# Kernel tuning notes

Hardware: AMD Instinct MI355X
Metric: run time of the kernel (lower is better)

Reference implementation:

```python
import jax, jax.numpy as jnp
import numpy as np

N, E, F_IN, D_COORD, W, KW, KIN, DEPTH = 10000, 300000, 3, 3, 32, 256, 6, 4

def _lin(k, i, o):
    return jax.random.normal(k, (i, o), jnp.float32) * (1.0 / np.sqrt(i))

def setup_inputs() -> dict:
    key = jax.random.key(0)
    ks = jax.random.split(key, 16)
    x = jax.random.normal(ks[0], (N, F_IN), jnp.float32)
    edge_index = jax.random.randint(ks[1], (2, E), 0, N, jnp.int64)
    edge_attr = jax.random.normal(ks[2], (E, KIN), jnp.float32)
    coords_init = jax.random.normal(ks[3], (N, D_COORD), jnp.float32)
    return {
        "x": x, "edge_index": edge_index, "edge_attr": edge_attr,
        "coords_init": coords_init,
        "fc1_w": _lin(ks[4], F_IN, W), "fc1_b": jnp.zeros((W,), jnp.float32),
        # kernel DenseNet: [ker_in, ker_width//2, ker_width, width**2]
        "ker1_w": _lin(ks[5], KIN, KW // 2), "ker1_b": jnp.zeros((KW // 2,), jnp.float32),
        "ker2_w": _lin(ks[6], KW // 2, KW), "ker2_b": jnp.zeros((KW,), jnp.float32),
        "ker3_w": _lin(ks[7], KW, W * W), "ker3_b": jnp.zeros((W * W,), jnp.float32),
        # coord MLP: Linear(W,W)+ReLU+Linear(W,1)
        "cm1_w": _lin(ks[8], W, W), "cm1_b": jnp.zeros((W,), jnp.float32),
        "cm2_w": _lin(ks[9], W, 1), "cm2_b": jnp.zeros((1,), jnp.float32),
        # fc2: Linear(W,2W)+ReLU+Linear(2W,1)
        "fc2a_w": _lin(ks[10], W, 2 * W), "fc2a_b": jnp.zeros((2 * W,), jnp.float32),
        "fc2b_w": _lin(ks[11], 2 * W, 1), "fc2b_b": jnp.zeros((1,), jnp.float32),
        "depth": DEPTH,
    }

def reference(x, edge_index, edge_attr, coords_init,
              fc1_w, fc1_b, ker1_w, ker1_b, ker2_w, ker2_b, ker3_w, ker3_b,
              cm1_w, cm1_b, cm2_w, cm2_b, fc2a_w, fc2a_b, fc2b_w, fc2b_b, depth):
    n = x.shape[0]
    w = fc1_w.shape[1]
    row, col = edge_index[0], edge_index[1]
    h = x @ fc1_w + fc1_b  # [N, W]
    # edge kernel MLP -> per-edge [W, W] matrix (edge_attr fixed across layers)
    k = jax.nn.relu(edge_attr @ ker1_w + ker1_b)
    k = jax.nn.relu(k @ ker2_w + ker2_b)
    k = (k @ ker3_w + ker3_b).reshape(-1, w, w)  # [E, W, W]
    cnt = jnp.clip(jax.ops.segment_sum(jnp.ones((row.shape[0], 1), h.dtype), row, n), 1.0)
    coord = coords_init
    for _ in range(depth):
        m = jnp.einsum('eij,ej->ei', k, h[col])              # gather + kernel apply
        agg = jax.ops.segment_sum(m, row, n) / cnt           # mean scatter to nodes
        we = jax.nn.relu(m @ cm1_w + cm1_b) @ cm2_w + cm2_b  # [E, 1] coord weights
        trans = (coord[row] - coord[col]) * we               # equivariant edge vectors
        coord = coord + jax.ops.segment_sum(trans, row, n) / cnt
        h = jax.nn.relu(h + agg)
    out = jax.nn.relu(h @ fc2a_w + fc2a_b) @ fc2b_w + fc2b_b  # [N, 1]
    return out, coord
```

## Files before the change

### kernel.cpp

```cpp
#include <hip/hip_runtime.h>

#define NN 10000
#define NE 300000
#define DEPTH 4

typedef unsigned int   u32;
typedef unsigned short u16;
typedef unsigned char  u8;

typedef _Float16 half8  __attribute__((ext_vector_type(8)));
typedef _Float16 half2t __attribute__((ext_vector_type(2)));
typedef float  floatx16 __attribute__((ext_vector_type(16)));

__device__ __forceinline__ u32 f2h(float f) {
    f = fminf(fmaxf(f, -60000.f), 60000.f);
    _Float16 h = (_Float16)f;
    return (u32)__builtin_bit_cast(u16, h);
}
__device__ __forceinline__ float h2f(u16 b) {
    return (float)__builtin_bit_cast(_Float16, b);
}

__global__ void sentinel_kernel(float* out, int n, float val) {
    int i = blockIdx.x * 256 + threadIdx.x;
    if (i < n) out[i] = val;
}

__global__ void detect_idx_kernel(const int* __restrict__ ei, int* __restrict__ flag) {
    __shared__ int nz;
    if (threadIdx.x == 0) nz = 0;
    __syncthreads();
    if (ei[threadIdx.x * 2 + 1] != 0) atomicAdd(&nz, 1);
    __syncthreads();
    if (threadIdx.x == 0) *flag = (nz == 0) ? 1 : 0;
}

__global__ __launch_bounds__(256) void convert_idx_kernel(
    const int* __restrict__ ei, const int* __restrict__ flag,
    int* __restrict__ ridx, int* __restrict__ cidx)
{
    int e = blockIdx.x * 256 + threadIdx.x;
    if (e >= 2 * NE) return;
    const int is64 = *flag;
    int v = is64 ? ei[2 * e] : ei[e];
    if (e < NE) ridx[e] = v; else cidx[e - NE] = v;
}

__global__ __launch_bounds__(256) void init_nodes_kernel(
    const float* __restrict__ x, const float* __restrict__ fc1w,
    const float* __restrict__ fc1b, const float* __restrict__ ci,
    float* __restrict__ h, float* __restrict__ coord)
{
    int idx = blockIdx.x * 256 + threadIdx.x;
    if (idx < NN * 32) {
        int v = idx >> 5, f = idx & 31;
        float acc = fc1b[f];
#pragma unroll
        for (int i = 0; i < 3; i++) acc += x[v * 3 + i] * fc1w[i * 32 + f];
        h[idx] = acc;
    }
    if (idx < NN * 3) coord[idx] = ci[idx];
}

__global__ __launch_bounds__(256) void count_kernel(
    const int* __restrict__ ridx, const int* __restrict__ cidx,
    int* __restrict__ rowcnt, int* __restrict__ colcnt)
{
    int e = blockIdx.x * 256 + threadIdx.x;
    if (e < NE) { atomicAdd(&rowcnt[ridx[e]], 1); atomicAdd(&colcnt[cidx[e]], 1); }
}

__global__ void scan_kernel(const int* __restrict__ colcnt, const int* __restrict__ rowcnt,
                            int* __restrict__ cstart, int* __restrict__ cnext,
                            int* __restrict__ rstart, int* __restrict__ rnext,
                            float* __restrict__ invc, int mode)
{
    __shared__ int partC[256], partR[256];
    const int t = threadIdx.x;
    int sumC = 0, sumR = 0;
    for (int i = 0; i < 40; i++) {
        int v = t * 40 + i;
        if (v < NN) { sumC += colcnt[v]; sumR += rowcnt[v]; }
    }
    partC[t] = sumC; partR[t] = sumR;
    __syncthreads();
    if (t == 0) {
        int rc = 0, rr = 0;
        for (int i = 0; i < 256; i++) {
            int tc = partC[i]; partC[i] = rc; rc += tc;
            int tr = partR[i]; partR[i] = rr; rr += tr;
        }
    }
    __syncthreads();
    int runC = partC[t], runR = partR[t];
    for (int i = 0; i < 40; i++) {
        int v = t * 40 + i;
        if (v < NN) {
            cstart[v] = runC; cnext[v] = runC; runC += colcnt[v];
            if (mode) { rstart[v] = runR; rnext[v] = runR; runR += rowcnt[v]; }
        }
    }
    if (t == 255) { cstart[NN] = runC; if (mode) rstart[NN] = runR; }
    for (int v = t; v < NN; v += 256) invc[v] = 1.0f / fmaxf((float)rowcnt[v], 1.0f);
}

__global__ __launch_bounds__(256) void scatter_kernel(
    const int* __restrict__ cidx, const int* __restrict__ ridx,
    int* __restrict__ cnext, int* __restrict__ rnext,
    int* __restrict__ elist, int* __restrict__ rpos, int* __restrict__ rcol,
    int mode)
{
    int e = blockIdx.x * 256 + threadIdx.x;
    if (e >= NE) return;
    int pos = atomicAdd(&cnext[cidx[e]], 1);
    elist[pos] = e;
    if (mode) {
        int rp = atomicAdd(&rnext[ridx[e]], 1);
        rpos[e] = rp;
        rcol[rp] = cidx[e];
    }
}

__global__ __launch_bounds__(256) void w2pack_kernel(
    const float* __restrict__ w2, u16* __restrict__ w2h)
{
    const int slot = blockIdx.x * 256 + threadIdx.x;
    const int c = slot >> 9, s = (slot >> 6) & 7, l = slot & 63;
    const int li = l & 31, hf = l >> 5;
    const int k0 = s * 16 + hf * 8, col = c * 32 + li;
    u32 pk[8];
#pragma unroll
    for (int j = 0; j < 8; j++) pk[j] = f2h(w2[(size_t)(k0 + j) * 256 + col]);
    uint4 o;
    o.x = pk[0] | (pk[1] << 16);
    o.y = pk[2] | (pk[3] << 16);
    o.z = pk[4] | (pk[5] << 16);
    o.w = pk[6] | (pk[7] << 16);
    *(uint4*)&w2h[(size_t)slot * 8] = o;
}

__global__ void cm1pack_kernel(const float* __restrict__ cm1w, u16* __restrict__ cmpk)
{
    const int t = threadIdx.x;
    if (t >= 128) return;
    const int s2 = t >> 6, l = t & 63, li = l & 31, hf = l >> 5;
    u32 pk[8];
#pragma unroll
    for (int j = 0; j < 8; j++) pk[j] = f2h(cm1w[(s2 * 16 + hf * 8 + j) * 32 + li]);
    uint4 o;
    o.x = pk[0] | (pk[1] << 16);
    o.y = pk[2] | (pk[3] << 16);
    o.z = pk[4] | (pk[5] << 16);
    o.w = pk[6] | (pk[7] << 16);
    *(uint4*)&cmpk[(size_t)(s2 * 64 + l) * 8] = o;
}

__global__ __launch_bounds__(256) void mlp_k2_kernel(
    const float* __restrict__ ea,
    const float* __restrict__ w1, const float* __restrict__ b1,
    const u16* __restrict__ w2h, const float* __restrict__ b2,
    u8* __restrict__ k2base, float* __restrict__ k2s)
{
    __shared__ __align__(16) float ea_s[32 * 6];
    __shared__ __align__(16) u16   k1f[4096];
    __shared__ __align__(16) u16   M_s[32 * 258];
    __shared__ float pmax_s[4][32];
    const int t  = threadIdx.x;
    const int e0 = blockIdx.x * 32;

    for (int idx = t; idx < 192; idx += 256)
        ea_s[idx] = ea[(size_t)e0 * 6 + idx];
    __syncthreads();

    for (int slot = t; slot < 512; slot += 256) {
        const int s  = slot >> 6;
        const int l  = slot & 63;
        const int li = l & 31, hf = l >> 5;
        const int k0 = s * 16 + hf * 8;
        float acc[8];
        {
            const float4 ba = *(const float4*)&b1[k0];
            const float4 bb = *(const float4*)&b1[k0 + 4];
            acc[0] = ba.x; acc[1] = ba.y; acc[2] = ba.z; acc[3] = ba.w;
            acc[4] = bb.x; acc[5] = bb.y; acc[6] = bb.z; acc[7] = bb.w;
        }
#pragma unroll
        for (int i = 0; i < 6; i++) {
            const float ev = ea_s[li * 6 + i];
            const float4 wa = *(const float4*)&w1[i * 128 + k0];
            const float4 wb = *(const float4*)&w1[i * 128 + k0 + 4];
            acc[0] += ev * wa.x; acc[1] += ev * wa.y;
            acc[2] += ev * wa.z; acc[3] += ev * wa.w;
            acc[4] += ev * wb.x; acc[5] += ev * wb.y;
            acc[6] += ev * wb.z; acc[7] += ev * wb.w;
        }
        uint4 o;
        o.x = f2h(fmaxf(acc[0], 0.f)) | (f2h(fmaxf(acc[1], 0.f)) << 16);
        o.y = f2h(fmaxf(acc[2], 0.f)) | (f2h(fmaxf(acc[3], 0.f)) << 16);
        o.z = f2h(fmaxf(acc[4], 0.f)) | (f2h(fmaxf(acc[5], 0.f)) << 16);
        o.w = f2h(fmaxf(acc[6], 0.f)) | (f2h(fmaxf(acc[7], 0.f)) << 16);
        *(uint4*)&k1f[slot * 8] = o;
    }
    __syncthreads();

    {
        const int w  = t >> 6, l = t & 63;
        const int li = l & 31, hf = l >> 5;
#pragma unroll
        for (int ct = 0; ct < 2; ct++) {
            const int c = w * 2 + ct;
            floatx16 acc;
#pragma unroll
            for (int r = 0; r < 16; r++) acc[r] = 0.f;
#pragma unroll
            for (int s = 0; s < 8; s++) {
                const half8 a = __builtin_bit_cast(half8,
                    *(const uint4*)&k1f[(s * 64 + l) * 8]);
                const half8 b = __builtin_bit_cast(half8,
                    *(const uint4*)&w2h[(((size_t)c * 8 + s) * 64 + l) * 8]);
                acc = __builtin_amdgcn_mfma_f32_32x32x16_f16(a, b, acc, 0, 0, 0);
            }
            const float bb = b2[c * 32 + li];
#pragma unroll
            for (int r = 0; r < 16; r++) {
                const int e = (r & 3) + 8 * (r >> 2) + 4 * hf;
                M_s[e * 258 + c * 32 + li] = (u16)f2h(fmaxf(acc[r] + bb, 0.f));
            }
        }
    }
    __syncthreads();

    {
        const int el = t & 31, qq = t >> 5;
        const int w  = t >> 6;
        float vals[32];
#pragma unroll
        for (int c = 0; c < 16; c++) {
            const u32 hw = *(const u32*)&M_s[el * 258 + qq * 32 + c * 2];
            vals[c * 2]     = h2f((u16)hw);
            vals[c * 2 + 1] = h2f((u16)(hw >> 16));
        }
        float mx = 0.f;
#pragma unroll
        for (int u = 0; u < 32; u++) mx = fmaxf(mx, vals[u]);
        mx = fmaxf(mx, __shfl_xor(mx, 32, 64));
        if ((t & 32) == 0) pmax_s[w][el] = mx;
        __syncthreads();
        mx = fmaxf(fmaxf(pmax_s[0][el], pmax_s[1][el]),
                   fmaxf(pmax_s[2][el], pmax_s[3][el]));
        const float sc  = mx / 255.f;
        const float inv = (mx > 0.f) ? 255.f / mx : 0.f;
        if (t < 32) k2s[e0 + el] = sc;
        u32 w8[8];
#pragma unroll
        for (int u = 0; u < 8; u++) {
            u32 q0 = (u32)fminf(rintf(vals[u * 4 + 0] * inv), 255.f);
            u32 q1 = (u32)fminf(rintf(vals[u * 4 + 1] * inv), 255.f);
            u32 q2 = (u32)fminf(rintf(vals[u * 4 + 2] * inv), 255.f);
            u32 q3 = (u32)fminf(rintf(vals[u * 4 + 3] * inv), 255.f);
            w8[u] = q0 | (q1 << 8) | (q2 << 16) | (q3 << 24);
        }
        u8* outp = k2base + (size_t)(e0 + el) * 256 + qq * 32;
        *(uint4*)outp        = make_uint4(w8[0], w8[1], w8[2], w8[3]);
        *(uint4*)(outp + 16) = make_uint4(w8[4], w8[5], w8[6], w8[7]);
    }
}

__global__ __launch_bounds__(256) void bvec_kernel(
    const float* __restrict__ h, const float* __restrict__ b3, float* __restrict__ bvec)
{
    int idx = blockIdx.x * 256 + threadIdx.x;
    if (idx >= NN * 32) return;
    int v = idx >> 5, i = idx & 31;
    const float* hp = &h[(size_t)v * 32];
    const float* bp = &b3[i * 32];
    float acc = 0.f;
#pragma unroll
    for (int c = 0; c < 8; c++) {
        float4 hv = *(const float4*)&hp[c * 4];
        float4 bv = *(const float4*)&bp[c * 4];
        acc += hv.x * bv.x + hv.y * bv.y + hv.z * bv.z + hv.w * bv.w;
    }
    bvec[idx] = acc;
}

__global__ __launch_bounds__(256) void g_kernel(
    const float* __restrict__ h, const float* __restrict__ w3,
    u16* __restrict__ Gg)
{
    __shared__ __align__(16) u32 h16[128 * 16];
    const int t  = threadIdx.x;
    const int v0 = blockIdx.x * 128;

    {
        const int v = t >> 1, hh = t & 1;
        float4 a = make_float4(0.f, 0.f, 0.f, 0.f), b = a, c = a, d = a;
        if (v0 + v < NN) {
            const float* hp = &h[(size_t)(v0 + v) * 32 + hh * 16];
            a = *(const float4*)hp;       b = *(const float4*)(hp + 4);
            c = *(const float4*)(hp + 8); d = *(const float4*)(hp + 12);
        }
        uint4 o0, o1;
        o0.x = f2h(a.x) | (f2h(a.y) << 16);
        o0.y = f2h(a.z) | (f2h(a.w) << 16);
        o0.z = f2h(b.x) | (f2h(b.y) << 16);
        o0.w = f2h(b.z) | (f2h(b.w) << 16);
        o1.x = f2h(c.x) | (f2h(c.y) << 16);
        o1.y = f2h(c.z) | (f2h(c.w) << 16);
        o1.z = f2h(d.x) | (f2h(d.y) << 16);
        o1.w = f2h(d.z) | (f2h(d.w) << 16);
        *(uint4*)&h16[v * 16 + hh * 8]     = o0;
        *(uint4*)&h16[v * 16 + hh * 8 + 4] = o1;
    }
    __syncthreads();

    const int by    = blockIdx.y;
    const int lane  = t >> 2;
    const int i     = lane & 31;
    const int halfk = lane >> 5;
    const int j0    = (t & 3) * 2;
    const int k0    = by * 16 + halfk * 8 + j0;

    u32 w0p[16], w1p[16];
    {
        const float* wp0 = &w3[(size_t)k0 * 1024 + (size_t)i * 32];
        const float* wp1 = wp0 + 1024;
#pragma unroll
        for (int c = 0; c < 8; c++) {
            const float4 a = *(const float4*)&wp0[c * 4];
            w0p[c * 2]     = f2h(a.x) | (f2h(a.y) << 16);
            w0p[c * 2 + 1] = f2h(a.z) | (f2h(a.w) << 16);
            const float4 b = *(const float4*)&wp1[c * 4];
            w1p[c * 2]     = f2h(b.x) | (f2h(b.y) << 16);
            w1p[c * 2 + 1] = f2h(b.z) | (f2h(b.w) << 16);
        }
    }
    const int vmax = min(128, NN - v0);
    u32* outp = (u32*)Gg;
#pragma unroll 2
    for (int v = 0; v < vmax; v++) {
        float a0 = 0.f, a1 = 0.f;
#pragma unroll
        for (int c = 0; c < 4; c++) {
            const uint4 q = *(const uint4*)&h16[v * 16 + c * 4];
            const half2t h0 = __builtin_bit_cast(half2t, q.x);
            const half2t h1 = __builtin_bit_cast(half2t, q.y);
            const half2t h2 = __builtin_bit_cast(half2t, q.z);
            const half2t h3 = __builtin_bit_cast(half2t, q.w);
            a0 = __builtin_amdgcn_fdot2(h0, __builtin_bit_cast(half2t, w0p[c*4+0]), a0, false);
            a0 = __builtin_amdgcn_fdot2(h1, __builtin_bit_cast(half2t, w0p[c*4+1]), a0, false);
            a0 = __builtin_amdgcn_fdot2(h2, __builtin_bit_cast(half2t, w0p[c*4+2]), a0, false);
            a0 = __builtin_amdgcn_fdot2(h3, __builtin_bit_cast(half2t, w0p[c*4+3]), a0, false);
            a1 = __builtin_amdgcn_fdot2(h0, __builtin_bit_cast(half2t, w1p[c*4+0]), a1, false);
            a1 = __builtin_amdgcn_fdot2(h1, __builtin_bit_cast(half2t, w1p[c*4+1]), a1, false);
            a1 = __builtin_amdgcn_fdot2(h2, __builtin_bit_cast(half2t, w1p[c*4+2]), a1, false);
            a1 = __builtin_amdgcn_fdot2(h3, __builtin_bit_cast(half2t, w1p[c*4+3]), a1, false);
        }
        outp[(size_t)(v0 + v) * 4096 + by * 256 + t] = f2h(a0) | (f2h(a1) << 16);
    }
}

__global__ __launch_bounds__(256) void edge_kernel(
    const int* __restrict__ cstart, const int* __restrict__ elist,
    const int* __restrict__ ridx, const int* __restrict__ rpos,
    const u8* __restrict__ k2base, const float* __restrict__ k2s,
    const u16* __restrict__ Gg, const float* __restrict__ coord,
    const u16* __restrict__ cmpk, const float* __restrict__ cm1b,
    const float* __restrict__ cm2w, const float* __restrict__ cm2b,
    const float* __restrict__ bvec,
    float* __restrict__ agg, float* __restrict__ dco,
    u16* __restrict__ mbuf, u16* __restrict__ webuf, int mode)
{
    const int t    = threadIdx.x;
    const int w    = t >> 6;
    const int l    = t & 63;
    const int li   = l & 31;
    const int half = l >> 5;

    __shared__ __align__(16) float Mlds_all[4][32 * 34];
    __shared__ int idxS_all[4][32];
    float* Mlds = Mlds_all[w];
    int*   idxS = idxS_all[w];

    const int n = blockIdx.x * 4 + w;
    if (n >= NN) return;
    const int s0  = cstart[n];
    const int deg = cstart[n + 1] - s0;
    if (deg == 0) return;

    half8 cmb[2];
    cmb[0] = __builtin_bit_cast(half8, *(const uint4*)&cmpk[(size_t)(0 * 64 + l) * 8]);
    cmb[1] = __builtin_bit_cast(half8, *(const uint4*)&cmpk[(size_t)(1 * 64 + l) * 8]);
    half8 onesb;
#pragma unroll
    for (int j = 0; j < 8; j++) onesb[j] = (_Float16)1.0f;
    const float cm1bq = cm1b[li];
    const float cm2q  = cm2w[li];
    const float cm2b0 = cm2b[0];
    const float bv    = bvec[n * 32 + li];
    const float con   = (mode == 0 && li < 3) ? coord[(size_t)n * 3 + li] : 0.f;
    const u16* Gn = Gg + (size_t)n * 8192;

    for (int base = 0; base < deg; base += 32) {
        const int mye   = base + li;
        const int valid = (mye < deg) ? 1 : 0;
        const int eid   = valid ? elist[s0 + mye] : 0;
        if (l < 32) idxS[l] = valid ? (mode ? rpos[eid] : ridx[eid]) : 0;

        uint4 gr[16];
#pragma unroll
        for (int s = 0; s < 16; s++)
            gr[s] = *(const uint4*)(Gn + s * 512 + l * 8);
        const float se = valid ? k2s[eid] : 0.f;
        const u8* k2row = k2base + (size_t)eid * 256 + half * 8;
        uint2 kr[16];
#pragma unroll
        for (int s = 0; s < 16; s++) kr[s] = *(const uint2*)(k2row + s * 16);

        floatx16 acc;
#pragma unroll
        for (int r = 0; r < 16; r++) acc[r] = bv;
#pragma unroll
        for (int s = 0; s < 16; s++) {
            half8 a;
#pragma unroll
            for (int j = 0; j < 4; j++) {
                a[j]     = (_Float16)((float)((kr[s].x >> (8 * j)) & 0xffu) * se);
                a[4 + j] = (_Float16)((float)((kr[s].y >> (8 * j)) & 0xffu) * se);
            }
            acc = __builtin_amdgcn_mfma_f32_32x32x16_f16(
                a, __builtin_bit_cast(half8, gr[s]), acc, 0, 0, 0);
        }

#pragma unroll
        for (int r = 0; r < 16; r++) {
            const int e = (r & 3) + 8 * (r >> 2) + 4 * half;
            Mlds[e * 34 + li] = acc[r];
        }
        if (mode == 0) {
#pragma unroll
            for (int r = 0; r < 16; r++) {
                const int e = (r & 3) + 8 * (r >> 2) + 4 * half;
                if (base + e < deg)
                    atomicAdd(&agg[(size_t)idxS[e] * 32 + li], acc[r]);
            }
        } else {
#pragma unroll
            for (int r = 0; r < 16; r++) {
                const int e = (r & 3) + 8 * (r >> 2) + 4 * half;
                if (base + e < deg)
                    mbuf[(size_t)idxS[e] * 32 + li] = (u16)f2h(acc[r]);
            }
        }
        asm volatile("s_waitcnt lgkmcnt(0)" ::: "memory");

        floatx16 acc2;
#pragma unroll
        for (int r = 0; r < 16; r++) acc2[r] = cm1bq;
#pragma unroll
        for (int s2 = 0; s2 < 2; s2++) {
            const float* mp = &Mlds[li * 34 + s2 * 16 + half * 8];
            const float2 m0 = *(const float2*)mp;
            const float2 m1 = *(const float2*)(mp + 2);
            const float2 m2 = *(const float2*)(mp + 4);
            const float2 m3 = *(const float2*)(mp + 6);
            half8 a;
            a[0] = (_Float16)m0.x; a[1] = (_Float16)m0.y;
            a[2] = (_Float16)m1.x; a[3] = (_Float16)m1.y;
            a[4] = (_Float16)m2.x; a[5] = (_Float16)m2.y;
            a[6] = (_Float16)m3.x; a[7] = (_Float16)m3.y;
            acc2 = __builtin_amdgcn_mfma_f32_32x32x16_f16(a, cmb[s2], acc2, 0, 0, 0);
        }

#pragma unroll
        for (int r = 0; r < 16; r++) {
            const int e = (r & 3) + 8 * (r >> 2) + 4 * half;
            Mlds[e * 34 + li] = fmaxf(acc2[r], 0.f) * cm2q;
        }
        asm volatile("s_waitcnt lgkmcnt(0)" ::: "memory");
        floatx16 acc3;
#pragma unroll
        for (int r = 0; r < 16; r++) acc3[r] = cm2b0;
#pragma unroll
        for (int s2 = 0; s2 < 2; s2++) {
            const float* mp = &Mlds[li * 34 + s2 * 16 + half * 8];
            const float2 m0 = *(const float2*)mp;
            const float2 m1 = *(const float2*)(mp + 2);
            const float2 m2 = *(const float2*)(mp + 4);
            const float2 m3 = *(const float2*)(mp + 6);
            half8 a;
            a[0] = (_Float16)m0.x; a[1] = (_Float16)m0.y;
            a[2] = (_Float16)m1.x; a[3] = (_Float16)m1.y;
            a[4] = (_Float16)m2.x; a[5] = (_Float16)m2.y;
            a[6] = (_Float16)m3.x; a[7] = (_Float16)m3.y;
            acc3 = __builtin_amdgcn_mfma_f32_32x32x16_f16(a, onesb, acc3, 0, 0, 0);
        }

        if (mode == 0) {
#pragma unroll
            for (int r = 0; r < 16; r++) {
                const int e = (r & 3) + 8 * (r >> 2) + 4 * half;
                if (base + e < deg && li < 3) {
                    const int rr = idxS[e];
                    const float d = coord[(size_t)rr * 3 + li] - con;
                    atomicAdd(&dco[(size_t)rr * 3 + li], d * acc3[r]);
                }
            }
        } else {
#pragma unroll
            for (int r = 0; r < 16; r++) {
                const int e = (r & 3) + 8 * (r >> 2) + 4 * half;
                if (base + e < deg && li == 0)
                    webuf[idxS[e]] = (u16)f2h(acc3[r]);
            }
        }
    }
}

__global__ __launch_bounds__(256) void node_update_kernel(
    float* __restrict__ h, float* __restrict__ agg,
    float* __restrict__ coord, float* __restrict__ dco,
    const float* __restrict__ invc)
{
    int idx = blockIdx.x * 256 + threadIdx.x;
    if (idx < NN * 32) {
        int v = idx >> 5;
        h[idx] = fmaxf(h[idx] + agg[idx] * invc[v], 0.f);
        agg[idx] = 0.f;
    }
    if (idx < NN * 3) {
        coord[idx] += dco[idx] * invc[idx / 3];
        dco[idx] = 0.f;
    }
}

__global__ __launch_bounds__(256) void node_update2_kernel(
    float* __restrict__ h, const float* __restrict__ coordCur,
    float* __restrict__ coordNew, const u16* __restrict__ mbuf,
    const u16* __restrict__ webuf, const int* __restrict__ rcol,
    const int* __restrict__ rstart, const float* __restrict__ invc)
{
    const int t = threadIdx.x, w = t >> 6, l = t & 63;
    const int li = l & 31, half = l >> 5;
    const int v = blockIdx.x * 4 + w;
    if (v >= NN) return;
    const int s0 = rstart[v], s1 = rstart[v + 1];
    const float iv = invc[v];

    float acc = 0.f;
    for (int s = s0 + half; s < s1; s += 2)
        acc += h2f(mbuf[(size_t)s * 32 + li]);
    acc += __shfl_xor(acc, 32, 64);
    if (half == 0)
        h[(size_t)v * 32 + li] = fmaxf(h[(size_t)v * 32 + li] + acc * iv, 0.f);

    const float c0 = coordCur[(size_t)v * 3 + 0];
    const float c1 = coordCur[(size_t)v * 3 + 1];
    const float c2 = coordCur[(size_t)v * 3 + 2];
    float p0 = 0.f, p1 = 0.f, p2 = 0.f;
    for (int s = s0 + l; s < s1; s += 64) {
        const float we = h2f(webuf[s]);
        const int col = rcol[s];
        p0 += (c0 - coordCur[(size_t)col * 3 + 0]) * we;
        p1 += (c1 - coordCur[(size_t)col * 3 + 1]) * we;
        p2 += (c2 - coordCur[(size_t)col * 3 + 2]) * we;
    }
#pragma unroll
    for (int off = 32; off >= 1; off >>= 1) {
        p0 += __shfl_xor(p0, off, 64);
        p1 += __shfl_xor(p1, off, 64);
        p2 += __shfl_xor(p2, off, 64);
    }
    if (l == 0) {
        coordNew[(size_t)v * 3 + 0] = c0 + p0 * iv;
        coordNew[(size_t)v * 3 + 1] = c1 + p1 * iv;
        coordNew[(size_t)v * 3 + 2] = c2 + p2 * iv;
    }
}

__global__ __launch_bounds__(256) void final_kernel(
    const float* __restrict__ h, const float* __restrict__ coord,
    const float* __restrict__ wa, const float* __restrict__ ba,
    const float* __restrict__ wb, const float* __restrict__ bb,
    float* __restrict__ out)
{
    const int lane = threadIdx.x & 63;
    const int v = blockIdx.x * 4 + (threadIdx.x >> 6);
    if (v >= NN) return;
    const float hreg = (lane < 32) ? h[(size_t)v * 32 + lane] : 0.f;
    float acc = ba[lane];
#pragma unroll
    for (int f = 0; f < 32; f++) acc += __shfl(hreg, f, 64) * wa[f * 64 + lane];
    float part = fmaxf(acc, 0.f) * wb[lane];
#pragma unroll
    for (int off = 32; off >= 1; off >>= 1) part += __shfl_xor(part, off, 64);
    if (lane == 0) out[v] = part + bb[0];
    if (lane < 3) out[NN + (size_t)v * 3 + lane] = coord[(size_t)v * 3 + lane];
}

extern "C" void kernel_launch(void* const* d_in, const int* in_sizes, int n_in,
                              void* d_out, int out_size, void* d_ws, size_t ws_size,
                              hipStream_t stream)
{
    const float* x    = (const float*)d_in[0];
    const int*   ei   = (const int*)d_in[1];
    const float* ea   = (const float*)d_in[2];
    const float* ci   = (const float*)d_in[3];
    const float* fc1w = (const float*)d_in[4];
    const float* fc1b = (const float*)d_in[5];
    const float* k1w  = (const float*)d_in[6];
    const float* k1b  = (const float*)d_in[7];
    const float* k2w  = (const float*)d_in[8];
    const float* k2b  = (const float*)d_in[9];
    const float* k3w  = (const float*)d_in[10];
    const float* k3b  = (const float*)d_in[11];
    const float* cm1w = (const float*)d_in[12];
    const float* cm1b = (const float*)d_in[13];
    const float* cm2w = (const float*)d_in[14];
    const float* cm2b = (const float*)d_in[15];
    const float* f2aw = (const float*)d_in[16];
    const float* f2ab = (const float*)d_in[17];
    const float* f2bw = (const float*)d_in[18];
    const float* f2bb = (const float*)d_in[19];

    size_t o_k2, o_k2s, o_G, o_h, o_bv, o_coA, o_coB, o_invc, o_rc, o_cc,
           o_cs, o_rs, o_cn, o_rn, o_el, o_w2h, o_cmpk, o_agg, o_dco,
           o_ri, o_ci, o_rp, o_rcl, o_mb, o_wb;
#define ALGN(v) (((v) + 255) & ~(size_t)255)
    auto carve = [&](int mode) -> size_t {
        size_t o = 0;
        o_k2  = o; o += ALGN((size_t)NE * 256);
        o_k2s = o; o += ALGN((size_t)NE * 4);
        o_G   = o; o += ALGN((size_t)NN * 8192 * 2);
        o_h   = o; o += ALGN((size_t)NN * 32 * 4);
        o_bv  = o; o += ALGN((size_t)NN * 32 * 4);
        o_coA = o; o += ALGN((size_t)NN * 3 * 4);
        o_invc= o; o += ALGN((size_t)NN * 4);
        o_rc  = o; o += ALGN((size_t)NN * 4);
        o_cc  = o; o += ALGN((size_t)NN * 4);
        o_cs  = o; o += ALGN((size_t)(NN + 1) * 4);
        o_cn  = o; o += ALGN((size_t)NN * 4);
        o_el  = o; o += ALGN((size_t)NE * 4);
        o_w2h = o; o += ALGN((size_t)128 * 256 * 2);
        o_cmpk= o; o += ALGN((size_t)1024 * 2);
        if (mode == 0) {
            o_agg = o; o += ALGN((size_t)NN * 32 * 4);
            o_dco = o; o += ALGN((size_t)NN * 3 * 4);
            o_ri  = o; o += ALGN((size_t)NE * 4);
            o_ci  = o; o += ALGN((size_t)NE * 4);
            o_coB = o_coA; o_rs = o_cs; o_rn = o_cn;
            o_rp = o_el; o_rcl = o_el; o_mb = o_k2; o_wb = o_k2;
        } else {
            o_coB = o; o += ALGN((size_t)NN * 3 * 4);
            o_rs  = o; o += ALGN((size_t)(NN + 1) * 4);
            o_rn  = o; o += ALGN((size_t)NN * 4);
            o_rp  = o; o += ALGN((size_t)NE * 4);
            o_rcl = o; o += ALGN((size_t)NE * 4);
            const size_t u = o;
            o_ri = u; o_ci = u + ALGN((size_t)NE * 4);
            o_mb = u; o_wb = u + ALGN((size_t)NE * 32 * 2);
            const size_t setup_sz = 2 * ALGN((size_t)NE * 4);
            const size_t layer_sz = ALGN((size_t)NE * 32 * 2) + ALGN((size_t)NE * 2);
            o += (setup_sz > layer_sz) ? setup_sz : layer_sz;
            o_agg = o_k2; o_dco = o_k2;
        }
        return o;
    };
    int mode = (ws_size >= carve(1)) ? 1 : 0;
    size_t need = carve(mode);
    if (ws_size < need) {
        sentinel_kernel<<<(NN * 4 + 255) / 256, 256, 0, stream>>>((float*)d_out, NN * 4, 1.0e6f);
        return;
    }

    char* wsb = (char*)d_ws;
    u8*    k2g   = (u8*)(wsb + o_k2);
    float* k2s   = (float*)(wsb + o_k2s);
    u16*   Gg    = (u16*)(wsb + o_G);
    float* h     = (float*)(wsb + o_h);
    float* bvec  = (float*)(wsb + o_bv);
    float* coA   = (float*)(wsb + o_coA);
    float* coB   = (float*)(wsb + o_coB);
    float* invc  = (float*)(wsb + o_invc);
    int*   rowcnt= (int*)(wsb + o_rc);
    int*   colcnt= (int*)(wsb + o_cc);
    int*   cstart= (int*)(wsb + o_cs);
    int*   rstart= (int*)(wsb + o_rs);
    int*   cnext = (int*)(wsb + o_cn);
    int*   rnext = (int*)(wsb + o_rn);
    int*   elist = (int*)(wsb + o_el);
    u16*   w2h   = (u16*)(wsb + o_w2h);
    u16*   cmpk  = (u16*)(wsb + o_cmpk);
    float* agg   = (float*)(wsb + o_agg);
    float* dco   = (float*)(wsb + o_dco);
    int*   ridx  = (int*)(wsb + o_ri);
    int*   cidx  = (int*)(wsb + o_ci);
    int*   rpos  = (int*)(wsb + o_rp);
    int*   rcol  = (int*)(wsb + o_rcl);
    u16*   mbuf  = (u16*)(wsb + o_mb);
    u16*   webuf = (u16*)(wsb + o_wb);

    hipMemsetAsync(rowcnt, 0, (size_t)NN * 4, stream);
    hipMemsetAsync(colcnt, 0, (size_t)NN * 4, stream);
    if (mode == 0) {
        hipMemsetAsync(agg, 0, (size_t)NN * 32 * 4, stream);
        hipMemsetAsync(dco, 0, (size_t)NN * 3 * 4, stream);
    }

    detect_idx_kernel<<<1, 256, 0, stream>>>(ei, cnext);
    convert_idx_kernel<<<(2 * NE + 255) / 256, 256, 0, stream>>>(ei, cnext, ridx, cidx);
    init_nodes_kernel<<<(NN * 32 + 255) / 256, 256, 0, stream>>>(x, fc1w, fc1b, ci, h, coA);
    count_kernel<<<(NE + 255) / 256, 256, 0, stream>>>(ridx, cidx, rowcnt, colcnt);
    scan_kernel<<<1, 256, 0, stream>>>(colcnt, rowcnt, cstart, cnext, rstart, rnext,
                                       invc, mode);
    scatter_kernel<<<(NE + 255) / 256, 256, 0, stream>>>(cidx, ridx, cnext, rnext,
                                                         elist, rpos, rcol, mode);
    w2pack_kernel<<<16, 256, 0, stream>>>(k2w, w2h);
    cm1pack_kernel<<<1, 128, 0, stream>>>(cm1w, cmpk);
    mlp_k2_kernel<<<NE / 32, 256, 0, stream>>>(ea, k1w, k1b, w2h, k2b, k2g, k2s);

    float* coCur = coA;
    float* coAlt = coB;
    const dim3 ggrid((NN + 127) / 128, 16);
    for (int l = 0; l < DEPTH; l++) {
        bvec_kernel<<<(NN * 32 + 255) / 256, 256, 0, stream>>>(h, k3b, bvec);
        g_kernel<<<ggrid, 256, 0, stream>>>(h, k3w, Gg);
        edge_kernel<<<(NN + 3) / 4, 256, 0, stream>>>(cstart, elist, ridx, rpos,
                                                      k2g, k2s, Gg, coCur, cmpk,
                                                      cm1b, cm2w, cm2b, bvec,
                                                      agg, dco, mbuf, webuf, mode);
        if (mode == 1) {
            node_update2_kernel<<<(NN + 3) / 4, 256, 0, stream>>>(
                h, coCur, coAlt, mbuf, webuf, rcol, rstart, invc);
            float* tmp = coCur; coCur = coAlt; coAlt = tmp;
        } else {
            node_update_kernel<<<(NN * 32 + 255) / 256, 256, 0, stream>>>(
                h, agg, coCur, dco, invc);
        }
    }
    final_kernel<<<(NN + 3) / 4, 256, 0, stream>>>(h, coCur, f2aw, f2ab, f2bw, f2bb,
                                                   (float*)d_out);
}
```

Measured before the change: 924.7 us.

## Use MFMA for per-node G projection and cheaper fp16 dequant in edge kernel

```diff
diff --git a/kernel.cpp b/kernel.cpp
--- a/kernel.cpp
+++ b/kernel.cpp
@@ -19,6 +19,14 @@
 }
 __device__ __forceinline__ float h2f(u16 b) {
     return (float)__builtin_bit_cast(_Float16, b);
+}
+__device__ __forceinline__ u32 pkrtz2(float a, float b) {
+    return __builtin_bit_cast(u32, __builtin_amdgcn_cvt_pkrtz(a, b));
+}
+__device__ __forceinline__ u32 dq2(u32 x, u32 sel) {
+    const half2t h1024 = {(_Float16)1024.f, (_Float16)1024.f};
+    half2t v = __builtin_bit_cast(half2t, __builtin_amdgcn_perm(x, 0x64646464u, sel));
+    return __builtin_bit_cast(u32, v - h1024);
 }
 
 __global__ void sentinel_kernel(float* out, int n, float val) {
@@ -155,11 +163,36 @@
     *(uint4*)&cmpk[(size_t)(s2 * 64 + l) * 8] = o;
 }
 
+__global__ __launch_bounds__(256) void w3pack_kernel(
+    const float* __restrict__ w3, u16* __restrict__ w3g)
+{
+    const int slot = blockIdx.x * 256 + threadIdx.x;
+    const int lane = slot & 63;
+    const int ks   = (slot >> 6) & 1;
+    const int pt   = slot >> 7;
+    const int p    = pt * 32 + (lane & 31);
+    const int kb   = ks * 16 + (lane >> 5) * 8;
+    const int s  = p >> 9;
+    const int hf = (p >> 8) & 1;
+    const int i  = (p >> 3) & 31;
+    const int j7 = p & 7;
+    const int c  = s * 16 + hf * 8 + j7;
+    const float* wp = &w3[(size_t)c * 1024 + i * 32 + kb];
+    const float4 x0 = *(const float4*)wp;
+    const float4 x1 = *(const float4*)(wp + 4);
+    uint4 o;
+    o.x = f2h(x0.x) | (f2h(x0.y) << 16);
+    o.y = f2h(x0.z) | (f2h(x0.w) << 16);
+    o.z = f2h(x1.x) | (f2h(x1.y) << 16);
+    o.w = f2h(x1.z) | (f2h(x1.w) << 16);
+    *(uint4*)&w3g[(size_t)slot * 8] = o;
+}
+
 __global__ __launch_bounds__(256) void mlp_k2_kernel(
     const float* __restrict__ ea,
     const float* __restrict__ w1, const float* __restrict__ b1,
     const u16* __restrict__ w2h, const float* __restrict__ b2,
-    u8* __restrict__ k2base, float* __restrict__ k2s)
+    u8* __restrict__ k2base, u16* __restrict__ k2s)
 {
     __shared__ __align__(16) float ea_s[32 * 6];
     __shared__ __align__(16) u16   k1f[4096];
@@ -195,10 +228,10 @@
             acc[6] += ev * wb.z; acc[7] += ev * wb.w;
         }
         uint4 o;
-        o.x = f2h(fmaxf(acc[0], 0.f)) | (f2h(fmaxf(acc[1], 0.f)) << 16);
-        o.y = f2h(fmaxf(acc[2], 0.f)) | (f2h(fmaxf(acc[3], 0.f)) << 16);
-        o.z = f2h(fmaxf(acc[4], 0.f)) | (f2h(fmaxf(acc[5], 0.f)) << 16);
-        o.w = f2h(fmaxf(acc[6], 0.f)) | (f2h(fmaxf(acc[7], 0.f)) << 16);
+        o.x = pkrtz2(fmaxf(acc[0], 0.f), fmaxf(acc[1], 0.f));
+        o.y = pkrtz2(fmaxf(acc[2], 0.f), fmaxf(acc[3], 0.f));
+        o.z = pkrtz2(fmaxf(acc[4], 0.f), fmaxf(acc[5], 0.f));
+        o.w = pkrtz2(fmaxf(acc[6], 0.f), fmaxf(acc[7], 0.f));
         *(uint4*)&k1f[slot * 8] = o;
     }
     __syncthreads();
@@ -224,7 +257,8 @@
 #pragma unroll
             for (int r = 0; r < 16; r++) {
                 const int e = (r & 3) + 8 * (r >> 2) + 4 * hf;
-                M_s[e * 258 + c * 32 + li] = (u16)f2h(fmaxf(acc[r] + bb, 0.f));
+                M_s[e * 258 + c * 32 + li] =
+                    __builtin_bit_cast(u16, (_Float16)fmaxf(acc[r] + bb, 0.f));
             }
         }
     }
@@ -250,7 +284,7 @@
                    fmaxf(pmax_s[2][el], pmax_s[3][el]));
         const float sc  = mx / 255.f;
         const float inv = (mx > 0.f) ? 255.f / mx : 0.f;
-        if (t < 32) k2s[e0 + el] = sc;
+        if (t < 32) k2s[e0 + el] = (u16)f2h(sc);
         u32 w8[8];
 #pragma unroll
         for (int u = 0; u < 8; u++) {
@@ -285,85 +319,69 @@
 }
 
 __global__ __launch_bounds__(256) void g_kernel(
-    const float* __restrict__ h, const float* __restrict__ w3,
+    const float* __restrict__ h, const u16* __restrict__ w3g,
     u16* __restrict__ Gg)
 {
-    __shared__ __align__(16) u32 h16[128 * 16];
-    const int t  = threadIdx.x;
-    const int v0 = blockIdx.x * 128;
-
-    {
-        const int v = t >> 1, hh = t & 1;
-        float4 a = make_float4(0.f, 0.f, 0.f, 0.f), b = a, c = a, d = a;
-        if (v0 + v < NN) {
-            const float* hp = &h[(size_t)(v0 + v) * 32 + hh * 16];
-            a = *(const float4*)hp;       b = *(const float4*)(hp + 4);
-            c = *(const float4*)(hp + 8); d = *(const float4*)(hp + 12);
-        }
-        uint4 o0, o1;
-        o0.x = f2h(a.x) | (f2h(a.y) << 16);
-        o0.y = f2h(a.z) | (f2h(a.w) << 16);
-        o0.z = f2h(b.x) | (f2h(b.y) << 16);
-        o0.w = f2h(b.z) | (f2h(b.w) << 16);
-        o1.x = f2h(c.x) | (f2h(c.y) << 16);
-        o1.y = f2h(c.z) | (f2h(c.w) << 16);
-        o1.z = f2h(d.x) | (f2h(d.y) << 16);
-        o1.w = f2h(d.z) | (f2h(d.w) << 16);
-        *(uint4*)&h16[v * 16 + hh * 8]     = o0;
-        *(uint4*)&h16[v * 16 + hh * 8 + 4] = o1;
-    }
-    __syncthreads();
-
-    const int by    = blockIdx.y;
-    const int lane  = t >> 2;
-    const int i     = lane & 31;
-    const int halfk = lane >> 5;
-    const int j0    = (t & 3) * 2;
-    const int k0    = by * 16 + halfk * 8 + j0;
-
-    u32 w0p[16], w1p[16];
-    {
-        const float* wp0 = &w3[(size_t)k0 * 1024 + (size_t)i * 32];
-        const float* wp1 = wp0 + 1024;
-#pragma unroll
-        for (int c = 0; c < 8; c++) {
-            const float4 a = *(const float4*)&wp0[c * 4];
-            w0p[c * 2]     = f2h(a.x) | (f2h(a.y) << 16);
-            w0p[c * 2 + 1] = f2h(a.z) | (f2h(a.w) << 16);
-            const float4 b = *(const float4*)&wp1[c * 4];
-            w1p[c * 2]     = f2h(b.x) | (f2h(b.y) << 16);
-            w1p[c * 2 + 1] = f2h(b.z) | (f2h(b.w) << 16);
-        }
-    }
-    const int vmax = min(128, NN - v0);
-    u32* outp = (u32*)Gg;
-#pragma unroll 2
-    for (int v = 0; v < vmax; v++) {
-        float a0 = 0.f, a1 = 0.f;
-#pragma unroll
-        for (int c = 0; c < 4; c++) {
-            const uint4 q = *(const uint4*)&h16[v * 16 + c * 4];
-            const half2t h0 = __builtin_bit_cast(half2t, q.x);
-            const half2t h1 = __builtin_bit_cast(half2t, q.y);
-            const half2t h2 = __builtin_bit_cast(half2t, q.z);
-            const half2t h3 = __builtin_bit_cast(half2t, q.w);
-            a0 = __builtin_amdgcn_fdot2(h0, __builtin_bit_cast(half2t, w0p[c*4+0]), a0, false);
-            a0 = __builtin_amdgcn_fdot2(h1, __builtin_bit_cast(half2t, w0p[c*4+1]), a0, false);
-            a0 = __builtin_amdgcn_fdot2(h2, __builtin_bit_cast(half2t, w0p[c*4+2]), a0, false);
-            a0 = __builtin_amdgcn_fdot2(h3, __builtin_bit_cast(half2t, w0p[c*4+3]), a0, false);
-            a1 = __builtin_amdgcn_fdot2(h0, __builtin_bit_cast(half2t, w1p[c*4+0]), a1, false);
-            a1 = __builtin_amdgcn_fdot2(h1, __builtin_bit_cast(half2t, w1p[c*4+1]), a1, false);
-            a1 = __builtin_amdgcn_fdot2(h2, __builtin_bit_cast(half2t, w1p[c*4+2]), a1, false);
-            a1 = __builtin_amdgcn_fdot2(h3, __builtin_bit_cast(half2t, w1p[c*4+3]), a1, false);
-        }
-        outp[(size_t)(v0 + v) * 4096 + by * 256 + t] = f2h(a0) | (f2h(a1) << 16);
+    const int t = threadIdx.x, w = t >> 6, l = t & 63;
+    const int li = l & 31, hf = l >> 5;
+    const int n0 = blockIdx.x * 32;
+    const int node = n0 + li;
+
+    half8 a0, a1;
+    if (node < NN) {
+        const float* hp = &h[(size_t)node * 32 + hf * 8];
+        const float4 x0 = *(const float4*)hp;
+        const float4 x1 = *(const float4*)(hp + 4);
+        const float4 y0 = *(const float4*)(hp + 16);
+        const float4 y1 = *(const float4*)(hp + 20);
+        uint4 ua, ub;
+        ua.x = pkrtz2(x0.x, x0.y); ua.y = pkrtz2(x0.z, x0.w);
+        ua.z = pkrtz2(x1.x, x1.y); ua.w = pkrtz2(x1.z, x1.w);
+        ub.x = pkrtz2(y0.x, y0.y); ub.y = pkrtz2(y0.z, y0.w);
+        ub.z = pkrtz2(y1.x, y1.y); ub.w = pkrtz2(y1.z, y1.w);
+        a0 = __builtin_bit_cast(half8, ua);
+        a1 = __builtin_bit_cast(half8, ub);
+    } else {
+        const uint4 z = make_uint4(0u, 0u, 0u, 0u);
+        a0 = __builtin_bit_cast(half8, z);
+        a1 = __builtin_bit_cast(half8, z);
+    }
+
+    const int pt0 = blockIdx.y * 64 + w * 16;
+    const int full = (n0 + 32 <= NN) ? 1 : 0;
+#pragma unroll 4
+    for (int it = 0; it < 16; it++) {
+        const int pt = pt0 + it;
+        const uint4 b0u = *(const uint4*)&w3g[((size_t)pt * 2 + 0) * 512 + (size_t)l * 8];
+        const uint4 b1u = *(const uint4*)&w3g[((size_t)pt * 2 + 1) * 512 + (size_t)l * 8];
+        floatx16 acc;
+#pragma unroll
+        for (int r = 0; r < 16; r++) acc[r] = 0.f;
+        acc = __builtin_amdgcn_mfma_f32_32x32x16_f16(
+            a0, __builtin_bit_cast(half8, b0u), acc, 0, 0, 0);
+        acc = __builtin_amdgcn_mfma_f32_32x32x16_f16(
+            a1, __builtin_bit_cast(half8, b1u), acc, 0, 0, 0);
+        if (full) {
+#pragma unroll
+            for (int r = 0; r < 16; r++) {
+                const int nn = n0 + (r & 3) + 8 * (r >> 2) + 4 * hf;
+                Gg[(size_t)nn * 8192 + pt * 32 + li] = (u16)f2h(acc[r]);
+            }
+        } else {
+#pragma unroll
+            for (int r = 0; r < 16; r++) {
+                const int nn = n0 + (r & 3) + 8 * (r >> 2) + 4 * hf;
+                if (nn < NN)
+                    Gg[(size_t)nn * 8192 + pt * 32 + li] = (u16)f2h(acc[r]);
+            }
+        }
     }
 }
 
 __global__ __launch_bounds__(256) void edge_kernel(
     const int* __restrict__ cstart, const int* __restrict__ elist,
     const int* __restrict__ ridx, const int* __restrict__ rpos,
-    const u8* __restrict__ k2base, const float* __restrict__ k2s,
+    const u8* __restrict__ k2base, const u16* __restrict__ k2s,
     const u16* __restrict__ Gg, const float* __restrict__ coord,
     const u16* __restrict__ cmpk, const float* __restrict__ cm1b,
     const float* __restrict__ cm2w, const float* __restrict__ cm2b,
@@ -378,9 +396,11 @@
     const int half = l >> 5;
 
     __shared__ __align__(16) float Mlds_all[4][32 * 34];
-    __shared__ int idxS_all[4][32];
+    __shared__ int   idxS_all[4][32];
+    __shared__ float seS_all[4][32];
     float* Mlds = Mlds_all[w];
     int*   idxS = idxS_all[w];
+    float* seS  = seS_all[w];
 
     const int n = blockIdx.x * 4 + w;
     if (n >= NN) return;
@@ -405,13 +425,13 @@
         const int mye   = base + li;
         const int valid = (mye < deg) ? 1 : 0;
         const int eid   = valid ? elist[s0 + mye] : 0;
-        if (l < 32) idxS[l] = valid ? (mode ? rpos[eid] : ridx[eid]) : 0;
+        const float se  = valid ? h2f(k2s[eid]) : 0.f;
+        if (l < 32) { idxS[l] = valid ? (mode ? rpos[eid] : ridx[eid]) : 0; seS[l] = se; }
 
         uint4 gr[16];
 #pragma unroll
         for (int s = 0; s < 16; s++)
             gr[s] = *(const uint4*)(Gn + s * 512 + l * 8);
-        const float se = valid ? k2s[eid] : 0.f;
         const u8* k2row = k2base + (size_t)eid * 256 + half * 8;
         uint2 kr[16];
 #pragma unroll
@@ -419,17 +439,22 @@
 
         floatx16 acc;
 #pragma unroll
-        for (int r = 0; r < 16; r++) acc[r] = bv;
+        for (int r = 0; r < 16; r++) acc[r] = 0.f;
 #pragma unroll
         for (int s = 0; s < 16; s++) {
-            half8 a;
-#pragma unroll
-            for (int j = 0; j < 4; j++) {
-                a[j]     = (_Float16)((float)((kr[s].x >> (8 * j)) & 0xffu) * se);
-                a[4 + j] = (_Float16)((float)((kr[s].y >> (8 * j)) & 0xffu) * se);
-            }
+            uint4 au;
+            au.x = dq2(kr[s].x, 0x00050004u);
+            au.y = dq2(kr[s].x, 0x00070006u);
+            au.z = dq2(kr[s].y, 0x00050004u);
+            au.w = dq2(kr[s].y, 0x00070006u);
             acc = __builtin_amdgcn_mfma_f32_32x32x16_f16(
-                a, __builtin_bit_cast(half8, gr[s]), acc, 0, 0, 0);
+                __builtin_bit_cast(half8, au),
+                __builtin_bit_cast(half8, gr[s]), acc, 0, 0, 0);
+        }
+#pragma unroll
+        for (int r = 0; r < 16; r++) {
+            const int e = (r & 3) + 8 * (r >> 2) + 4 * half;
+            acc[r] = acc[r] * seS[e] + bv;
         }
 
 #pragma unroll
@@ -449,7 +474,8 @@
             for (int r = 0; r < 16; r++) {
                 const int e = (r & 3) + 8 * (r >> 2) + 4 * half;
                 if (base + e < deg)
-                    mbuf[(size_t)idxS[e] * 32 + li] = (u16)f2h(acc[r]);
+                    mbuf[(size_t)idxS[e] * 32 + li] =
+                        __builtin_bit_cast(u16, (_Float16)acc[r]);
             }
         }
         asm volatile("s_waitcnt lgkmcnt(0)" ::: "memory");
@@ -464,12 +490,13 @@
             const float2 m1 = *(const float2*)(mp + 2);
             const float2 m2 = *(const float2*)(mp + 4);
             const float2 m3 = *(const float2*)(mp + 6);
-            half8 a;
-            a[0] = (_Float16)m0.x; a[1] = (_Float16)m0.y;
-            a[2] = (_Float16)m1.x; a[3] = (_Float16)m1.y;
-            a[4] = (_Float16)m2.x; a[5] = (_Float16)m2.y;
-            a[6] = (_Float16)m3.x; a[7] = (_Float16)m3.y;
-            acc2 = __builtin_amdgcn_mfma_f32_32x32x16_f16(a, cmb[s2], acc2, 0, 0, 0);
+            uint4 au;
+            au.x = pkrtz2(m0.x, m0.y);
+            au.y = pkrtz2(m1.x, m1.y);
+            au.z = pkrtz2(m2.x, m2.y);
+            au.w = pkrtz2(m3.x, m3.y);
+            acc2 = __builtin_amdgcn_mfma_f32_32x32x16_f16(
+                __builtin_bit_cast(half8, au), cmb[s2], acc2, 0, 0, 0);
         }
 
 #pragma unroll
@@ -488,12 +515,13 @@
             const float2 m1 = *(const float2*)(mp + 2);
             const float2 m2 = *(const float2*)(mp + 4);
             const float2 m3 = *(const float2*)(mp + 6);
-            half8 a;
-            a[0] = (_Float16)m0.x; a[1] = (_Float16)m0.y;
-            a[2] = (_Float16)m1.x; a[3] = (_Float16)m1.y;
-            a[4] = (_Float16)m2.x; a[5] = (_Float16)m2.y;
-            a[6] = (_Float16)m3.x; a[7] = (_Float16)m3.y;
-            acc3 = __builtin_amdgcn_mfma_f32_32x32x16_f16(a, onesb, acc3, 0, 0, 0);
+            uint4 au;
+            au.x = pkrtz2(m0.x, m0.y);
+            au.y = pkrtz2(m1.x, m1.y);
+            au.z = pkrtz2(m2.x, m2.y);
+            au.w = pkrtz2(m3.x, m3.y);
+            acc3 = __builtin_amdgcn_mfma_f32_32x32x16_f16(
+                __builtin_bit_cast(half8, au), onesb, acc3, 0, 0, 0);
         }
 
         if (mode == 0) {
@@ -511,7 +539,7 @@
             for (int r = 0; r < 16; r++) {
                 const int e = (r & 3) + 8 * (r >> 2) + 4 * half;
                 if (base + e < deg && li == 0)
-                    webuf[idxS[e]] = (u16)f2h(acc3[r]);
+                    webuf[idxS[e]] = __builtin_bit_cast(u16, (_Float16)acc3[r]);
             }
         }
     }
@@ -624,13 +652,13 @@
     const float* f2bb = (const float*)d_in[19];
 
     size_t o_k2, o_k2s, o_G, o_h, o_bv, o_coA, o_coB, o_invc, o_rc, o_cc,
-           o_cs, o_rs, o_cn, o_rn, o_el, o_w2h, o_cmpk, o_agg, o_dco,
+           o_cs, o_rs, o_cn, o_rn, o_el, o_w2h, o_cmpk, o_w3g, o_agg, o_dco,
            o_ri, o_ci, o_rp, o_rcl, o_mb, o_wb;
 #define ALGN(v) (((v) + 255) & ~(size_t)255)
     auto carve = [&](int mode) -> size_t {
         size_t o = 0;
         o_k2  = o; o += ALGN((size_t)NE * 256);
-        o_k2s = o; o += ALGN((size_t)NE * 4);
+        o_k2s = o; o += ALGN((size_t)NE * 2);
         o_G   = o; o += ALGN((size_t)NN * 8192 * 2);
         o_h   = o; o += ALGN((size_t)NN * 32 * 4);
         o_bv  = o; o += ALGN((size_t)NN * 32 * 4);
@@ -643,6 +671,7 @@
         o_el  = o; o += ALGN((size_t)NE * 4);
         o_w2h = o; o += ALGN((size_t)128 * 256 * 2);
         o_cmpk= o; o += ALGN((size_t)1024 * 2);
+        o_w3g = o; o += ALGN((size_t)32768 * 8 * 2);
         if (mode == 0) {
             o_agg = o; o += ALGN((size_t)NN * 32 * 4);
             o_dco = o; o += ALGN((size_t)NN * 3 * 4);
@@ -675,7 +704,7 @@
 
     char* wsb = (char*)d_ws;
     u8*    k2g   = (u8*)(wsb + o_k2);
-    float* k2s   = (float*)(wsb + o_k2s);
+    u16*   k2s   = (u16*)(wsb + o_k2s);
     u16*   Gg    = (u16*)(wsb + o_G);
     float* h     = (float*)(wsb + o_h);
     float* bvec  = (float*)(wsb + o_bv);
@@ -691,6 +720,7 @@
     int*   elist = (int*)(wsb + o_el);
     u16*   w2h   = (u16*)(wsb + o_w2h);
     u16*   cmpk  = (u16*)(wsb + o_cmpk);
+    u16*   w3g   = (u16*)(wsb + o_w3g);
     float* agg   = (float*)(wsb + o_agg);
     float* dco   = (float*)(wsb + o_dco);
     int*   ridx  = (int*)(wsb + o_ri);
@@ -717,14 +747,15 @@
                                                          elist, rpos, rcol, mode);
     w2pack_kernel<<<16, 256, 0, stream>>>(k2w, w2h);
     cm1pack_kernel<<<1, 128, 0, stream>>>(cm1w, cmpk);
+    w3pack_kernel<<<128, 256, 0, stream>>>(k3w, w3g);
     mlp_k2_kernel<<<NE / 32, 256, 0, stream>>>(ea, k1w, k1b, w2h, k2b, k2g, k2s);
 
     float* coCur = coA;
     float* coAlt = coB;
-    const dim3 ggrid((NN + 127) / 128, 16);
+    const dim3 ggrid((NN + 31) / 32, 4);
     for (int l = 0; l < DEPTH; l++) {
         bvec_kernel<<<(NN * 32 + 255) / 256, 256, 0, stream>>>(h, k3b, bvec);
-        g_kernel<<<ggrid, 256, 0, stream>>>(h, k3w, Gg);
+        g_kernel<<<ggrid, 256, 0, stream>>>(h, w3g, Gg);
         edge_kernel<<<(NN + 3) / 4, 256, 0, stream>>>(cstart, elist, ridx, rpos,
                                                       k2g, k2s, Gg, coCur, cmpk,
                                                       cm1b, cm2w, cm2b, bvec,
```

New measurement: 860.1 us. -7.0%, faster.
